# Performance work log

Measured on AMD Instinct MI355X. Metric: run time of the kernel, lower is better.

Reference implementation:

```python
import jax, jax.numpy as jnp
import numpy as np

B, U1, U2 = 4, 2048, 2048
C = 256      # in_feat_dim
F = 256      # feat_dim
M = 4        # num_modes
D = C // M   # attention_mode_dim = 64
ATTN_CLIP = 500.0
LN_EPS = 1e-12


def setup_inputs() -> dict:
    key = jax.random.key(0)
    ks = jax.random.split(key, 8)
    s = 0.02  # base_initializer_range
    inp = {
        "query_feat": jax.random.normal(ks[0], (B, U1, C), jnp.float32),
        "key_feat": jax.random.normal(ks[1], (B, U2, C), jnp.float32),
        "Wq": jax.random.normal(ks[2], (M * D, C), jnp.float32) * s,
        "bq": jnp.zeros((M * D,), jnp.float32),
    }
    # tie_qk_scheme='shared': key linear shares query weights
    inp["Wk"] = inp["Wq"]
    inp["bk"] = inp["bq"]
    inp["Wv"] = jax.random.normal(ks[3], (M * F, C), jnp.float32) * s  # first_linear, v_has_bias=False
    inp["W_mid"] = jax.random.normal(ks[4], (F, F), jnp.float32) * s   # MMSharedMid shared_linear
    inp["b_mid"] = jnp.zeros((F,), jnp.float32)
    inp["W_out"] = jax.random.normal(ks[5], (M, F, F), jnp.float32) * s  # grouped 1x1 conv, per mode
    inp["b_out"] = jnp.zeros((M, F), jnp.float32)
    inp["ln_g"] = jnp.ones((F,), jnp.float32)   # resout LayerNorm
    inp["ln_b"] = jnp.zeros((F,), jnp.float32)
    inp["W_score"] = jax.random.normal(ks[6], (1, F), jnp.float32) * s  # LearnedSoftAggregate
    inp["b_score"] = jnp.zeros((1,), jnp.float32)
    return inp


def _layer_norm(x, g, b):
    mu = jnp.mean(x, axis=-1, keepdims=True)
    var = jnp.var(x, axis=-1, keepdims=True)
    return (x - mu) * jax.lax.rsqrt(var + LN_EPS) * g + b


def reference(query_feat, key_feat, Wq, bq, Wk, bk, Wv, W_mid, b_mid,
              W_out, b_out, ln_g, ln_b, W_score, b_score):
    # --- tied-QK multi-mode attention ---
    q = (query_feat @ Wq.T + bq).reshape(B, U1, M, D)
    k = (key_feat @ Wk.T + bk).reshape(B, U2, M, D)
    scores = jnp.einsum('bimd,bjmd->bmij', q, k) / jnp.sqrt(jnp.float32(D))
    scores = jnp.clip(scores, -ATTN_CLIP, ATTN_CLIP)  # attn_clip
    probs = jax.nn.softmax(scores, axis=-1)           # [B, M, U1, U2]

    # --- ExpandedFeatTrans: value projection + fusion ---
    v = (key_feat @ Wv.T).reshape(B, U2, M, F)        # first_linear (no bias)
    fused = jnp.einsum('bmij,bjmf->bmif', probs, v)   # [B, M, U1, F]

    # MMSharedMid: shared linear over F + gelu (dropout = identity in eval)
    mid = jax.nn.gelu(fused @ W_mid.T + b_mid, approximate=False)

    # MMPrivateOutput: per-mode grouped 1x1 conv; NOTE the original code computes
    # x_comb = x + shortcut but then layer-norms x (shortcut dropped) - kept faithful.
    out = jnp.einsum('bmif,mgf->bmig', mid, W_out) + b_out[None, :, None, :]
    out = _layer_norm(out, ln_g, ln_b)                # [B, M, U1, F]

    # LearnedSoftAggregate over modes (group_dim=1, keepdim=False)
    mode_scores = out @ W_score.T + b_score           # [B, M, U1, 1]
    mode_probs = jax.nn.softmax(mode_scores, axis=1)
    return jnp.sum(out * mode_probs, axis=1)          # [B, U1, F]
```

## Files before the change

kernel.cpp:

```cpp
#include <hip/hip_runtime.h>

typedef __attribute__((ext_vector_type(8))) short short8;
typedef __attribute__((ext_vector_type(4))) float f32x4;
typedef __attribute__((ext_vector_type(16))) float f32x16;
typedef unsigned short u16t;
typedef unsigned int u32t;

#define MFMA16(a, b, c) __builtin_amdgcn_mfma_f32_16x16x32_bf16((a), (b), (c), 0, 0, 0)
#define MFMA32(a, b, c) __builtin_amdgcn_mfma_f32_32x32x16_bf16((a), (b), (c), 0, 0, 0)

__device__ __forceinline__ u16t f2bf(float f) {
  u32t u = __float_as_uint(f);
  u32t r = u + 0x7fffu + ((u >> 16) & 1u);
  return (u16t)(r >> 16);
}
__device__ __forceinline__ float bf2f(u16t b) {
  return __uint_as_float(((u32t)b) << 16);
}
__device__ __forceinline__ short8 pack8(float4 a0, float4 a1) {
  short8 r;
  r[0] = (short)f2bf(a0.x); r[1] = (short)f2bf(a0.y);
  r[2] = (short)f2bf(a0.z); r[3] = (short)f2bf(a0.w);
  r[4] = (short)f2bf(a1.x); r[5] = (short)f2bf(a1.y);
  r[6] = (short)f2bf(a1.z); r[7] = (short)f2bf(a1.w);
  return r;
}
__device__ __forceinline__ u32t packrhu(float a, float b) {
  u32t ua = __float_as_uint(a) + 0x8000u;
  u32t ub = __float_as_uint(b) + 0x8000u;
  return (ua >> 16) | (ub & 0xffff0000u);
}

__device__ __forceinline__ void proj_dev(
    const float* __restrict__ A, const float* __restrict__ W,
    const float* __restrict__ bias, float scale,
    u16t* __restrict__ out, int mode, int bx, int by,
    u16t* As, u16t* Ws) {
  const int tid = threadIdx.x;
  const int w = tid >> 6, lane = tid & 63, quad = lane >> 4, l15 = lane & 15;
  const int l31 = lane & 31, h8 = (lane >> 5) * 8;
  const int rt = bx * 64;
  const int ct = by * 64;
  const int wrow = (w >> 1) * 32, wcol = (w & 1) * 32;
  const int r2 = tid >> 3, c8 = tid & 7;

  const f32x4 fzero = {0.f, 0.f, 0.f, 0.f};
  f32x4 acc[2][2];
#pragma unroll
  for (int i = 0; i < 2; i++)
#pragma unroll
    for (int j = 0; j < 2; j++) acc[i][j] = fzero;

  for (int kt = 0; kt < 4; ++kt) {
    __syncthreads();
#pragma unroll
    for (int hh = 0; hh < 2; ++hh) {
      int rr = r2 + hh * 32;
      const float4* pa = (const float4*)(A + (size_t)(rt + rr) * 256 + kt * 64 + c8 * 8);
      const float4* pw = (const float4*)(W + (size_t)(ct + rr) * 256 + kt * 64 + c8 * 8);
      float4 w0 = pw[0], w1 = pw[1];
      w0.x *= scale; w0.y *= scale; w0.z *= scale; w0.w *= scale;
      w1.x *= scale; w1.y *= scale; w1.z *= scale; w1.w *= scale;
      *(short8*)&As[rr * 72 + c8 * 8] = pack8(pa[0], pa[1]);
      *(short8*)&Ws[rr * 72 + c8 * 8] = pack8(w0, w1);
    }
    __syncthreads();
#pragma unroll
    for (int ks = 0; ks < 2; ++ks) {
      short8 af0 = *(const short8*)&As[(wrow + l15) * 72 + ks * 32 + quad * 8];
      short8 af1 = *(const short8*)&As[(wrow + 16 + l15) * 72 + ks * 32 + quad * 8];
      short8 bw0 = *(const short8*)&Ws[(wcol + l15) * 72 + ks * 32 + quad * 8];
      short8 bw1 = *(const short8*)&Ws[(wcol + 16 + l15) * 72 + ks * 32 + quad * 8];
      acc[0][0] = MFMA16(af0, bw0, acc[0][0]);
      acc[0][1] = MFMA16(af0, bw1, acc[0][1]);
      acc[1][0] = MFMA16(af1, bw0, acc[1][0]);
      acc[1][1] = MFMA16(af1, bw1, acc[1][1]);
    }
  }

  __syncthreads();
  u16t* Cs = As;
  if (mode == 0) {
#pragma unroll
    for (int i = 0; i < 2; i++) {
      int rl = wrow + i * 16 + quad * 4;
#pragma unroll
      for (int j = 0; j < 2; j++) {
        int cl = wcol + j * 16 + l15;
        float bv = bias ? bias[ct + cl] * scale : 0.f;
#pragma unroll
        for (int rg = 0; rg < 4; ++rg)
          Cs[(rl + rg) * 72 + cl] = f2bf(acc[i][j][rg] + bv);
      }
    }
  } else {
#pragma unroll
    for (int i = 0; i < 2; i++) {
      int rl = wrow + i * 16 + quad * 4;
#pragma unroll
      for (int j = 0; j < 2; j++) {
        int cl = wcol + j * 16 + l15;
        ushort4 pk;
        pk.x = f2bf(acc[i][j][0]);
        pk.y = f2bf(acc[i][j][1]);
        pk.z = f2bf(acc[i][j][2]);
        pk.w = f2bf(acc[i][j][3]);
        *(ushort4*)&Cs[cl * 72 + rl] = pk;
      }
    }
  }
  __syncthreads();

#pragma unroll
  for (int t2 = 0; t2 < 2; ++t2) {
    short8 frag = *(const short8*)&Cs[(t2 * 32 + l31) * 72 + w * 16 + h8];
    size_t base;
    if (mode == 0) {
      int b = rt >> 11, m = by;
      int it32 = ((rt & 2047) >> 5) + t2;
      base = (((size_t)(b * 4 + m) * 64 + it32) * 4 + w) * 512;
    } else {
      int b = rt >> 11, m = by >> 2;
      int fb = ((by & 3) << 1) + t2;
      int jt16 = ((rt & 2047) >> 4) + w;
      base = (((size_t)(b * 4 + m) * 8 + fb) * 128 + jt16) * 512;
    }
    *(short8*)(out + base + lane * 8) = frag;
  }
}

__global__ __launch_bounds__(256) void prep_kernel(
    const float* __restrict__ query, const float* __restrict__ key,
    const float* __restrict__ Wq, const float* __restrict__ bq,
    const float* __restrict__ Wv, const float* __restrict__ Wm,
    const float* __restrict__ Wo,
    u16t* __restrict__ WmB, u16t* __restrict__ WoB,
    u16t* __restrict__ QfB, u16t* __restrict__ KfB, u16t* __restrict__ VfB) {
  __shared__ __align__(16) u16t As[64 * 72];
  __shared__ __align__(16) u16t Ws[64 * 72];
  const int blk = blockIdx.x;
  const int tid = threadIdx.x;
  if (blk < 256) {
    int i = blk * 256 + tid;
    WmB[i] = f2bf(Wm[i]);
    return;
  }
  if (blk < 1280) {
    int i = (blk - 256) * 256 + tid;
    WoB[i] = f2bf(Wo[i]);
    return;
  }
  const float *A, *W, *bias;
  float scale;
  u16t* out;
  int mode, local;
  if (blk < 1792) {
    local = blk - 1280; A = query; W = Wq; bias = bq; scale = 0.125f; out = QfB; mode = 0;
  } else if (blk < 2304) {
    local = blk - 1792; A = key; W = Wq; bias = bq; scale = 1.0f; out = KfB; mode = 0;
  } else {
    local = blk - 2304; A = key; W = Wv; bias = nullptr; scale = 1.0f; out = VfB; mode = 1;
  }
  proj_dev(A, W, bias, scale, out, mode, local & 127, local >> 7, As, Ws);
}

__global__ __launch_bounds__(256, 3) void attn_kernel(
    const u16t* __restrict__ Qf, const u16t* __restrict__ Kf,
    const u16t* __restrict__ Vf,
    const u16t* __restrict__ Wmid, const u16t* __restrict__ Wout,
    const float* __restrict__ b_mid, const float* __restrict__ b_out,
    const float* __restrict__ ln_g, const float* __restrict__ ln_b,
    const float* __restrict__ Wsc, const float* __restrict__ b_sc,
    u16t* __restrict__ out_ln, float* __restrict__ scoresWS) {
  __shared__ __align__(16) u16t smF[32 * 264];
  __shared__ __align__(16) u16t smP[2][32 * 132];
  __shared__ float smL[128];
  __shared__ float smR[128];
  __shared__ float smS[64];
  const int tid = threadIdx.x;
  const int w = tid >> 6, lane = tid & 63, quad = lane >> 4, l15 = lane & 15;
  const int l31 = lane & 31, h = lane >> 5;
  const int L = blockIdx.x;
  const int xcd = L & 7, slot = L >> 3;
  const int bm = xcd * 2 + (slot >> 6);
  const int it32 = slot & 63;
  const int m = bm & 3;
  const int q0 = it32 * 32;

  const size_t lane8 = (size_t)lane * 8;

  const u16t* qbase = Qf + ((size_t)(bm * 64 + it32) * 4) * 512 + lane8;
  short8 qf4[4];
#pragma unroll
  for (int ksd = 0; ksd < 4; ++ksd)
    qf4[ksd] = *(const short8*)(qbase + ksd * 512);

  const u16t* kbase = Kf + ((size_t)bm * 256) * 512 + lane8;
  const u16t* vbase = Vf + ((size_t)(bm * 8 + 2 * w) * 128) * 512 + lane8;

  f32x16 facc[2];
#pragma unroll
  for (int j = 0; j < 2; j++)
#pragma unroll
    for (int r = 0; r < 16; r++) facc[j][r] = 0.f;
  float lsum = 0.f;

  short8 kf4[4];
#pragma unroll
  for (int ksd = 0; ksd < 4; ++ksd)
    kf4[ksd] = *(const short8*)(kbase + (size_t)w * 2048 + ksd * 512);

  {
    f32x16 sacc;
#pragma unroll
    for (int r = 0; r < 16; r++) sacc[r] = 0.f;
#pragma unroll
    for (int ksd = 0; ksd < 4; ++ksd)
      sacc = MFMA32(kf4[ksd], qf4[ksd], sacc);
    float ls = 0.f;
#pragma unroll
    for (int tt = 0; tt < 8; ++tt) {
      const int jl = ((2 * tt) & 3) + 8 * ((2 * tt) >> 2) + 4 * h;
      float p0 = __expf(sacc[2 * tt]);
      float p1 = __expf(sacc[2 * tt + 1]);
      ls += p0 + p1;
      *(u32t*)&smP[0][l31 * 132 + w * 32 + jl] = packrhu(p0, p1);
    }
    lsum += ls;
  }
#pragma unroll
  for (int ksd = 0; ksd < 4; ++ksd)
    kf4[ksd] = *(const short8*)(kbase + (size_t)(4 + w) * 2048 + ksd * 512);
  __syncthreads();

#pragma unroll 1
  for (int t = 0; t < 16; ++t) {
    u16t* Pb = &smP[t & 1][0];
    u16t* Pn = &smP[(t + 1) & 1][0];

    if (t < 15) {
      f32x16 sacc;
#pragma unroll
      for (int r = 0; r < 16; r++) sacc[r] = 0.f;
#pragma unroll
      for (int ksd = 0; ksd < 4; ++ksd)
        sacc = MFMA32(kf4[ksd], qf4[ksd], sacc);
      float ls = 0.f;
#pragma unroll
      for (int tt = 0; tt < 8; ++tt) {
        const int jl = ((2 * tt) & 3) + 8 * ((2 * tt) >> 2) + 4 * h;
        float p0 = __expf(sacc[2 * tt]);
        float p1 = __expf(sacc[2 * tt + 1]);
        ls += p0 + p1;
        *(u32t*)&Pn[l31 * 132 + w * 32 + jl] = packrhu(p0, p1);
      }
      lsum += ls;
    }
    if (t < 14) {
      const int jn = (t + 2) * 4 + w;
#pragma unroll
      for (int ksd = 0; ksd < 4; ++ksd)
        kf4[ksd] = *(const short8*)(kbase + (size_t)jn * 2048 + ksd * 512);
    }
#pragma unroll
    for (int jj = 0; jj < 4; ++jj) {
      short8 vf[2][2];
#pragma unroll
      for (int fb = 0; fb < 2; ++fb)
#pragma unroll
        for (int ks2 = 0; ks2 < 2; ++ks2)
          vf[fb][ks2] = *(const short8*)(vbase + ((size_t)fb * 128 + (t * 8 + jj * 2 + ks2)) * 512);
      short8 bbL[2];
#pragma unroll
      for (int ks2 = 0; ks2 < 2; ++ks2)
        bbL[ks2] = *(const short8*)&Pb[l31 * 132 + jj * 32 + ks2 * 16 + h * 8];
      facc[0] = MFMA32(vf[0][0], bbL[0], facc[0]);
      facc[0] = MFMA32(vf[0][1], bbL[1], facc[0]);
      facc[1] = MFMA32(vf[1][0], bbL[0], facc[1]);
      facc[1] = MFMA32(vf[1][1], bbL[1], facc[1]);
    }
    __syncthreads();
  }

  lsum += __shfl_xor(lsum, 32);
  if (h == 0) smL[w * 32 + l31] = lsum;
  __syncthreads();
  float inv = 1.f / (smL[l31] + smL[32 + l31] + smL[64 + l31] + smL[96 + l31]);

#pragma unroll
  for (int fb = 0; fb < 2; ++fb) {
#pragma unroll
    for (int g = 0; g < 4; ++g) {
      int fbase = w * 64 + fb * 32 + 8 * g + 4 * h;
      ushort4 pk4;
      pk4.x = f2bf(facc[fb][4 * g + 0] * inv);
      pk4.y = f2bf(facc[fb][4 * g + 1] * inv);
      pk4.z = f2bf(facc[fb][4 * g + 2] * inv);
      pk4.w = f2bf(facc[fb][4 * g + 3] * inv);
      *(ushort4*)&smF[l31 * 264 + fbase] = pk4;
    }
  }
  __syncthreads();

  const int rgrp = w >> 1, ch = w & 1;
  const int rowq = rgrp * 16 + quad * 4;
  const f32x4 fz4 = {0.f, 0.f, 0.f, 0.f};

  f32x4 macc[8];
#pragma unroll
  for (int i = 0; i < 8; i++) macc[i] = fz4;
  for (int kc = 0; kc < 8; ++kc) {
    short8 af = *(const short8*)&smF[(rgrp * 16 + l15) * 264 + kc * 32 + quad * 8];
#pragma unroll
    for (int nb = 0; nb < 8; ++nb) {
      short8 bw = *(const short8*)(Wmid + (size_t)(ch * 128 + nb * 16 + l15) * 256 + kc * 32 + quad * 8);
      macc[nb] = MFMA16(af, bw, macc[nb]);
    }
  }
#pragma unroll
  for (int nb = 0; nb < 8; ++nb) {
    int c = ch * 128 + nb * 16 + l15;
    float bmv = b_mid[c];
#pragma unroll
    for (int rg = 0; rg < 4; ++rg) {
      float x = macc[nb][rg] + bmv;
      macc[nb][rg] = 0.5f * x * (1.f + erff(x * 0.70710678118654752f));
    }
  }
  __syncthreads();
#pragma unroll
  for (int nb = 0; nb < 8; ++nb)
#pragma unroll
    for (int rg = 0; rg < 4; ++rg)
      smF[(rowq + rg) * 264 + ch * 128 + nb * 16 + l15] = f2bf(macc[nb][rg]);
  __syncthreads();

  const u16t* Wo = Wout + (size_t)m * 65536;
  f32x4 oacc[8];
#pragma unroll
  for (int i = 0; i < 8; i++) oacc[i] = fz4;
  for (int kc = 0; kc < 8; ++kc) {
    short8 af = *(const short8*)&smF[(rgrp * 16 + l15) * 264 + kc * 32 + quad * 8];
#pragma unroll
    for (int nb = 0; nb < 8; ++nb) {
      short8 bw = *(const short8*)(Wo + (size_t)(ch * 128 + nb * 16 + l15) * 256 + kc * 32 + quad * 8);
      oacc[nb] = MFMA16(af, bw, oacc[nb]);
    }
  }

  float sum[4] = {0, 0, 0, 0}, sq[4] = {0, 0, 0, 0};
#pragma unroll
  for (int nb = 0; nb < 8; ++nb) {
    int c = ch * 128 + nb * 16 + l15;
    float bo = b_out[m * 256 + c];
#pragma unroll
    for (int rg = 0; rg < 4; ++rg) {
      float x = oacc[nb][rg] + bo;
      oacc[nb][rg] = x;
      sum[rg] += x;
      sq[rg] += x * x;
    }
  }
#pragma unroll
  for (int rg = 0; rg < 4; ++rg) {
    float s = sum[rg], s2 = sq[rg];
    s += __shfl_xor(s, 1); s += __shfl_xor(s, 2); s += __shfl_xor(s, 4); s += __shfl_xor(s, 8);
    s2 += __shfl_xor(s2, 1); s2 += __shfl_xor(s2, 2); s2 += __shfl_xor(s2, 4); s2 += __shfl_xor(s2, 8);
    if (l15 == 0) {
      smR[(rowq + rg) + 32 * ch] = s;
      smR[64 + (rowq + rg) + 32 * ch] = s2;
    }
  }
  __syncthreads();
  float mu[4], rstd[4];
#pragma unroll
  for (int rg = 0; rg < 4; ++rg) {
    int r = rowq + rg;
    float s = smR[r] + smR[r + 32];
    float s2 = smR[64 + r] + smR[64 + r + 32];
    float mean = s * (1.f / 256.f);
    float var = s2 * (1.f / 256.f) - mean * mean;
    mu[rg] = mean;
    rstd[rg] = rsqrtf(var + 1e-12f);
  }

  float scp[4] = {0, 0, 0, 0};
#pragma unroll
  for (int nb = 0; nb < 8; ++nb) {
    int c = ch * 128 + nb * 16 + l15;
    float g = ln_g[c], bb2 = ln_b[c], wsv = Wsc[c];
#pragma unroll
    for (int rg = 0; rg < 4; ++rg) {
      float xn = (oacc[nb][rg] - mu[rg]) * rstd[rg] * g + bb2;
      out_ln[((size_t)bm * 2048 + (q0 + rowq + rg)) * 256 + c] = f2bf(xn);
      scp[rg] += xn * wsv;
    }
  }
#pragma unroll
  for (int rg = 0; rg < 4; ++rg) {
    float s = scp[rg];
    s += __shfl_xor(s, 1); s += __shfl_xor(s, 2); s += __shfl_xor(s, 4); s += __shfl_xor(s, 8);
    if (l15 == 0) smS[(rowq + rg) + 32 * ch] = s;
  }
  __syncthreads();
  if (ch == 0 && l15 == 0) {
#pragma unroll
    for (int rg = 0; rg < 4; ++rg) {
      int r = rowq + rg;
      scoresWS[bm * 2048 + q0 + r] = smS[r] + smS[r + 32] + b_sc[0];
    }
  }
}

__global__ __launch_bounds__(256) void agg_kernel(
    const u16t* __restrict__ out_ln, const float* __restrict__ scoresWS,
    float* __restrict__ out) {
  const int row = blockIdx.x;
  const int c = threadIdx.x;
  const int b = row >> 11, i = row & 2047;
  float s0 = scoresWS[(b * 4 + 0) * 2048 + i];
  float s1 = scoresWS[(b * 4 + 1) * 2048 + i];
  float s2 = scoresWS[(b * 4 + 2) * 2048 + i];
  float s3 = scoresWS[(b * 4 + 3) * 2048 + i];
  float mx = fmaxf(fmaxf(s0, s1), fmaxf(s2, s3));
  float e0 = __expf(s0 - mx), e1 = __expf(s1 - mx), e2 = __expf(s2 - mx), e3 = __expf(s3 - mx);
  float inv = 1.f / (e0 + e1 + e2 + e3);
  float acc = e0 * inv * bf2f(out_ln[((size_t)(b * 4 + 0) * 2048 + i) * 256 + c]) +
              e1 * inv * bf2f(out_ln[((size_t)(b * 4 + 1) * 2048 + i) * 256 + c]) +
              e2 * inv * bf2f(out_ln[((size_t)(b * 4 + 2) * 2048 + i) * 256 + c]) +
              e3 * inv * bf2f(out_ln[((size_t)(b * 4 + 3) * 2048 + i) * 256 + c]);
  out[(size_t)row * 256 + c] = acc;
}

extern "C" void kernel_launch(void* const* d_in, const int* in_sizes, int n_in,
                              void* d_out, int out_size, void* d_ws, size_t ws_size,
                              hipStream_t stream) {
  (void)in_sizes; (void)n_in; (void)out_size; (void)ws_size;
  const float* query = (const float*)d_in[0];
  const float* key   = (const float*)d_in[1];
  const float* Wq    = (const float*)d_in[2];
  const float* bq    = (const float*)d_in[3];
  const float* Wv    = (const float*)d_in[6];
  const float* Wm    = (const float*)d_in[7];
  const float* bmid  = (const float*)d_in[8];
  const float* Wo    = (const float*)d_in[9];
  const float* bo    = (const float*)d_in[10];
  const float* lng   = (const float*)d_in[11];
  const float* lnb   = (const float*)d_in[12];
  const float* Wsc   = (const float*)d_in[13];
  const float* bsc   = (const float*)d_in[14];

  char* p = (char*)d_ws;
  u16t* QfB = (u16t*)p; p += (size_t)2097152 * 2;
  u16t* KfB = (u16t*)p; p += (size_t)2097152 * 2;
  u16t* VfB = (u16t*)p; p += (size_t)8388608 * 2;
  u16t* WmB = (u16t*)p; p += (size_t)65536 * 2;
  u16t* WoB = (u16t*)p; p += (size_t)262144 * 2;
  u16t* outLn = (u16t*)p; p += (size_t)8388608 * 2;
  float* scWS = (float*)p; p += (size_t)32768 * 4;

  prep_kernel<<<4352, 256, 0, stream>>>(query, key, Wq, bq, Wv, Wm, Wo,
                                        WmB, WoB, QfB, KfB, VfB);

  attn_kernel<<<1024, 256, 0, stream>>>(QfB, KfB, VfB, WmB, WoB,
                                        bmid, bo, lng, lnb, Wsc, bsc,
                                        outLn, scWS);

  agg_kernel<<<8192, 256, 0, stream>>>(outLn, scWS, (float*)d_out);
}
```

Measured before the change: 237.3 us.

## Double query tile per block to 64 rows with 8 waves sharing V loads

The attention kernel now processes 64 query rows per block with 512 threads (8 waves) instead of 32 rows with 256 threads. Each V fragment loaded from global memory is reused across two 32-row halves of the probability tile, halving V traffic per query row. Shared memory and reduction arrays double, and the grid halves. The cost is fewer blocks, more shared memory per block, and a changed occupancy target that may limit latency hiding.

```diff
diff --git a/kernel.cpp b/kernel.cpp
--- a/kernel.cpp
+++ b/kernel.cpp
@@ -164,7 +164,7 @@
   proj_dev(A, W, bias, scale, out, mode, local & 127, local >> 7, As, Ws);
 }
 
-__global__ __launch_bounds__(256, 3) void attn_kernel(
+__global__ __launch_bounds__(512, 4) void attn_kernel(
     const u16t* __restrict__ Qf, const u16t* __restrict__ Kf,
     const u16t* __restrict__ Vf,
     const u16t* __restrict__ Wmid, const u16t* __restrict__ Wout,
@@ -172,31 +172,32 @@
     const float* __restrict__ ln_g, const float* __restrict__ ln_b,
     const float* __restrict__ Wsc, const float* __restrict__ b_sc,
     u16t* __restrict__ out_ln, float* __restrict__ scoresWS) {
-  __shared__ __align__(16) u16t smF[32 * 264];
-  __shared__ __align__(16) u16t smP[2][32 * 132];
-  __shared__ float smL[128];
-  __shared__ float smR[128];
-  __shared__ float smS[64];
+  __shared__ __align__(16) u16t smF[64 * 264];
+  __shared__ __align__(16) u16t smP[2][64 * 132];
+  __shared__ float smL[256];
+  __shared__ float smR[256];
+  __shared__ float smS[128];
   const int tid = threadIdx.x;
   const int w = tid >> 6, lane = tid & 63, quad = lane >> 4, l15 = lane & 15;
   const int l31 = lane & 31, h = lane >> 5;
   const int L = blockIdx.x;
   const int xcd = L & 7, slot = L >> 3;
-  const int bm = xcd * 2 + (slot >> 6);
-  const int it32 = slot & 63;
+  const int bm = xcd * 2 + (slot >> 5);
+  const int it64 = slot & 31;
   const int m = bm & 3;
-  const int q0 = it32 * 32;
+  const int q0 = it64 * 64;
+  const int jw = w & 3, ihS = w >> 2;
 
   const size_t lane8 = (size_t)lane * 8;
 
-  const u16t* qbase = Qf + ((size_t)(bm * 64 + it32) * 4) * 512 + lane8;
+  const u16t* qbase = Qf + ((size_t)(bm * 64 + it64 * 2 + ihS) * 4) * 512 + lane8;
   short8 qf4[4];
 #pragma unroll
   for (int ksd = 0; ksd < 4; ++ksd)
     qf4[ksd] = *(const short8*)(qbase + ksd * 512);
 
   const u16t* kbase = Kf + ((size_t)bm * 256) * 512 + lane8;
-  const u16t* vbase = Vf + ((size_t)(bm * 8 + 2 * w) * 128) * 512 + lane8;
+  const u16t* vbase = Vf + ((size_t)(bm * 8 + w) * 128) * 512 + lane8;
 
   f32x16 facc[2];
 #pragma unroll
@@ -208,7 +209,7 @@
   short8 kf4[4];
 #pragma unroll
   for (int ksd = 0; ksd < 4; ++ksd)
-    kf4[ksd] = *(const short8*)(kbase + (size_t)w * 2048 + ksd * 512);
+    kf4[ksd] = *(const short8*)(kbase + (size_t)jw * 2048 + ksd * 512);
 
   {
     f32x16 sacc;
@@ -224,13 +225,13 @@
       float p0 = __expf(sacc[2 * tt]);
       float p1 = __expf(sacc[2 * tt + 1]);
       ls += p0 + p1;
-      *(u32t*)&smP[0][l31 * 132 + w * 32 + jl] = packrhu(p0, p1);
+      *(u32t*)&smP[0][(ihS * 32 + l31) * 132 + jw * 32 + jl] = packrhu(p0, p1);
     }
     lsum += ls;
   }
 #pragma unroll
   for (int ksd = 0; ksd < 4; ++ksd)
-    kf4[ksd] = *(const short8*)(kbase + (size_t)(4 + w) * 2048 + ksd * 512);
+    kf4[ksd] = *(const short8*)(kbase + (size_t)(4 + jw) * 2048 + ksd * 512);
   __syncthreads();
 
 #pragma unroll 1
@@ -252,32 +253,23 @@
         float p0 = __expf(sacc[2 * tt]);
         float p1 = __expf(sacc[2 * tt + 1]);
         ls += p0 + p1;
-        *(u32t*)&Pn[l31 * 132 + w * 32 + jl] = packrhu(p0, p1);
+        *(u32t*)&Pn[(ihS * 32 + l31) * 132 + jw * 32 + jl] = packrhu(p0, p1);
       }
       lsum += ls;
     }
     if (t < 14) {
-      const int jn = (t + 2) * 4 + w;
+      const int jn = (t + 2) * 4 + jw;
 #pragma unroll
       for (int ksd = 0; ksd < 4; ++ksd)
         kf4[ksd] = *(const short8*)(kbase + (size_t)jn * 2048 + ksd * 512);
     }
 #pragma unroll
-    for (int jj = 0; jj < 4; ++jj) {
-      short8 vf[2][2];
-#pragma unroll
-      for (int fb = 0; fb < 2; ++fb)
-#pragma unroll
-        for (int ks2 = 0; ks2 < 2; ++ks2)
-          vf[fb][ks2] = *(const short8*)(vbase + ((size_t)fb * 128 + (t * 8 + jj * 2 + ks2)) * 512);
-      short8 bbL[2];
-#pragma unroll
-      for (int ks2 = 0; ks2 < 2; ++ks2)
-        bbL[ks2] = *(const short8*)&Pb[l31 * 132 + jj * 32 + ks2 * 16 + h * 8];
-      facc[0] = MFMA32(vf[0][0], bbL[0], facc[0]);
-      facc[0] = MFMA32(vf[0][1], bbL[1], facc[0]);
-      facc[1] = MFMA32(vf[1][0], bbL[0], facc[1]);
-      facc[1] = MFMA32(vf[1][1], bbL[1], facc[1]);
+    for (int ks = 0; ks < 8; ++ks) {
+      short8 vf = *(const short8*)(vbase + ((size_t)(t * 8 + ks)) * 512);
+      short8 b0 = *(const short8*)&Pb[l31 * 132 + ks * 16 + h * 8];
+      short8 b1 = *(const short8*)&Pb[(32 + l31) * 132 + ks * 16 + h * 8];
+      facc[0] = MFMA32(vf, b0, facc[0]);
+      facc[1] = MFMA32(vf, b1, facc[1]);
     }
     __syncthreads();
   }
@@ -285,19 +277,23 @@
   lsum += __shfl_xor(lsum, 32);
   if (h == 0) smL[w * 32 + l31] = lsum;
   __syncthreads();
-  float inv = 1.f / (smL[l31] + smL[32 + l31] + smL[64 + l31] + smL[96 + l31]);
-
-#pragma unroll
-  for (int fb = 0; fb < 2; ++fb) {
+  float inv[2];
+#pragma unroll
+  for (int ih = 0; ih < 2; ++ih)
+    inv[ih] = 1.f / (smL[(ih * 4 + 0) * 32 + l31] + smL[(ih * 4 + 1) * 32 + l31] +
+                     smL[(ih * 4 + 2) * 32 + l31] + smL[(ih * 4 + 3) * 32 + l31]);
+
+#pragma unroll
+  for (int ih = 0; ih < 2; ++ih) {
 #pragma unroll
     for (int g = 0; g < 4; ++g) {
-      int fbase = w * 64 + fb * 32 + 8 * g + 4 * h;
+      int fbase = w * 32 + 8 * g + 4 * h;
       ushort4 pk4;
-      pk4.x = f2bf(facc[fb][4 * g + 0] * inv);
-      pk4.y = f2bf(facc[fb][4 * g + 1] * inv);
-      pk4.z = f2bf(facc[fb][4 * g + 2] * inv);
-      pk4.w = f2bf(facc[fb][4 * g + 3] * inv);
-      *(ushort4*)&smF[l31 * 264 + fbase] = pk4;
+      pk4.x = f2bf(facc[ih][4 * g + 0] * inv[ih]);
+      pk4.y = f2bf(facc[ih][4 * g + 1] * inv[ih]);
+      pk4.z = f2bf(facc[ih][4 * g + 2] * inv[ih]);
+      pk4.w = f2bf(facc[ih][4 * g + 3] * inv[ih]);
+      *(ushort4*)&smF[(ih * 32 + l31) * 264 + fbase] = pk4;
     }
   }
   __syncthreads();
@@ -367,8 +363,8 @@
     s += __shfl_xor(s, 1); s += __shfl_xor(s, 2); s += __shfl_xor(s, 4); s += __shfl_xor(s, 8);
     s2 += __shfl_xor(s2, 1); s2 += __shfl_xor(s2, 2); s2 += __shfl_xor(s2, 4); s2 += __shfl_xor(s2, 8);
     if (l15 == 0) {
-      smR[(rowq + rg) + 32 * ch] = s;
-      smR[64 + (rowq + rg) + 32 * ch] = s2;
+      smR[(rowq + rg) + 64 * ch] = s;
+      smR[128 + (rowq + rg) + 64 * ch] = s2;
     }
   }
   __syncthreads();
@@ -376,8 +372,8 @@
 #pragma unroll
   for (int rg = 0; rg < 4; ++rg) {
     int r = rowq + rg;
-    float s = smR[r] + smR[r + 32];
-    float s2 = smR[64 + r] + smR[64 + r + 32];
+    float s = smR[r] + smR[r + 64];
+    float s2 = smR[128 + r] + smR[128 + r + 64];
     float mean = s * (1.f / 256.f);
     float var = s2 * (1.f / 256.f) - mean * mean;
     mu[rg] = mean;
@@ -400,14 +396,14 @@
   for (int rg = 0; rg < 4; ++rg) {
     float s = scp[rg];
     s += __shfl_xor(s, 1); s += __shfl_xor(s, 2); s += __shfl_xor(s, 4); s += __shfl_xor(s, 8);
-    if (l15 == 0) smS[(rowq + rg) + 32 * ch] = s;
+    if (l15 == 0) smS[(rowq + rg) + 64 * ch] = s;
   }
   __syncthreads();
   if (ch == 0 && l15 == 0) {
 #pragma unroll
     for (int rg = 0; rg < 4; ++rg) {
       int r = rowq + rg;
-      scoresWS[bm * 2048 + q0 + r] = smS[r] + smS[r + 32] + b_sc[0];
+      scoresWS[bm * 2048 + q0 + r] = smS[r] + smS[r + 64] + b_sc[0];
     }
   }
 }
@@ -462,9 +458,9 @@
   prep_kernel<<<4352, 256, 0, stream>>>(query, key, Wq, bq, Wv, Wm, Wo,
                                         WmB, WoB, QfB, KfB, VfB);
 
-  attn_kernel<<<1024, 256, 0, stream>>>(QfB, KfB, VfB, WmB, WoB,
-                                        bmid, bo, lng, lnb, Wsc, bsc,
-                                        outLn, scWS);
+  attn_kernel<<<512, 512, 0, stream>>>(QfB, KfB, VfB, WmB, WoB,
+                                       bmid, bo, lng, lnb, Wsc, bsc,
+                                       outLn, scWS);
 
   agg_kernel<<<8192, 256, 0, stream>>>(outLn, scWS, (float*)d_out);
 }
```

After: 281.8 us. 18.7% more time.

## Split weight conversion into own kernel and widen projection tiles to reuse activations

Applied to the files above, without the earlier changes.

Weight-to-bf16 conversion moves into a separate vectorized cvt kernel. The projection kernel now reads activation fragments straight from global memory into registers and reuses them across four 64-column output blocks, each block covering 256 columns. This cuts redundant activation loads and fp32-to-bf16 conversions and drops LDS staging in the main loop. It adds a kernel launch and more accumulator registers, and the attention kernel's launch bounds are raised to allow 4 blocks per CU.

```diff
diff --git a/kernel.cpp b/kernel.cpp
--- a/kernel.cpp
+++ b/kernel.cpp
@@ -31,140 +31,142 @@
   return (ua >> 16) | (ub & 0xffff0000u);
 }
 
-__device__ __forceinline__ void proj_dev(
-    const float* __restrict__ A, const float* __restrict__ W,
-    const float* __restrict__ bias, float scale,
-    u16t* __restrict__ out, int mode, int bx, int by,
-    u16t* As, u16t* Ws) {
+__global__ __launch_bounds__(256) void cvt_kernel(
+    const float* __restrict__ Wq, const float* __restrict__ Wv,
+    const float* __restrict__ Wm, const float* __restrict__ Wo,
+    u16t* __restrict__ WqB, u16t* __restrict__ WvB,
+    u16t* __restrict__ WmB, u16t* __restrict__ WoB) {
+  const int blk = blockIdx.x, tid = threadIdx.x;
+  const float* src; u16t* dst; int base;
+  if (blk < 64)       { src = Wq; dst = WqB; base = blk * 1024; }
+  else if (blk < 320) { src = Wv; dst = WvB; base = (blk - 64) * 1024; }
+  else if (blk < 384) { src = Wm; dst = WmB; base = (blk - 320) * 1024; }
+  else                { src = Wo; dst = WoB; base = (blk - 384) * 1024; }
+  int i = base + tid * 4;
+  float4 v = *(const float4*)(src + i);
+  ushort4 o;
+  o.x = f2bf(v.x); o.y = f2bf(v.y); o.z = f2bf(v.z); o.w = f2bf(v.w);
+  *(ushort4*)(dst + i) = o;
+}
+
+__global__ __launch_bounds__(256, 4) void proj_kernel(
+    const float* __restrict__ query, const float* __restrict__ key,
+    const u16t* __restrict__ WqB, const u16t* __restrict__ WvB,
+    const float* __restrict__ bq,
+    u16t* __restrict__ QfB, u16t* __restrict__ KfB, u16t* __restrict__ VfB) {
+  __shared__ __align__(16) u16t Cs[64 * 72];
   const int tid = threadIdx.x;
   const int w = tid >> 6, lane = tid & 63, quad = lane >> 4, l15 = lane & 15;
   const int l31 = lane & 31, h8 = (lane >> 5) * 8;
+  const int wrow = (w >> 1) * 32, wcol = (w & 1) * 32;
+
+  const float* A; const u16t* W16; const float* bias;
+  float ascale; u16t* out; int mode, bx, byg;
+  const int blk = blockIdx.x;
+  if (blk < 128) {
+    A = query; W16 = WqB; bias = bq; ascale = 0.125f; out = QfB; mode = 0; bx = blk; byg = 0;
+  } else if (blk < 256) {
+    A = key; W16 = WqB; bias = bq; ascale = 1.0f; out = KfB; mode = 0; bx = blk - 128; byg = 0;
+  } else {
+    int v2 = blk - 256;
+    A = key; W16 = WvB; bias = nullptr; ascale = 1.0f; out = VfB; mode = 1;
+    bx = v2 & 127; byg = v2 >> 7;
+  }
   const int rt = bx * 64;
-  const int ct = by * 64;
-  const int wrow = (w >> 1) * 32, wcol = (w & 1) * 32;
-  const int r2 = tid >> 3, c8 = tid & 7;
-
-  const f32x4 fzero = {0.f, 0.f, 0.f, 0.f};
-  f32x4 acc[2][2];
-#pragma unroll
-  for (int i = 0; i < 2; i++)
-#pragma unroll
-    for (int j = 0; j < 2; j++) acc[i][j] = fzero;
-
-  for (int kt = 0; kt < 4; ++kt) {
+
+  const f32x4 fz = {0.f, 0.f, 0.f, 0.f};
+  f32x4 acc[4][2][2];
+#pragma unroll
+  for (int n = 0; n < 4; n++)
+#pragma unroll
+    for (int i = 0; i < 2; i++)
+#pragma unroll
+      for (int j = 0; j < 2; j++) acc[n][i][j] = fz;
+
+  const float* arow0 = A + (size_t)(rt + wrow + l15) * 256;
+  const float* arow1 = A + (size_t)(rt + wrow + 16 + l15) * 256;
+  const u16t* wbase = W16 + (size_t)(byg * 256 + wcol + l15) * 256;
+
+#pragma unroll
+  for (int ks = 0; ks < 8; ++ks) {
+    const int kk = ks * 32 + quad * 8;
+    float4 a00 = *(const float4*)(arow0 + kk);
+    float4 a01 = *(const float4*)(arow0 + kk + 4);
+    float4 a10 = *(const float4*)(arow1 + kk);
+    float4 a11 = *(const float4*)(arow1 + kk + 4);
+    a00.x *= ascale; a00.y *= ascale; a00.z *= ascale; a00.w *= ascale;
+    a01.x *= ascale; a01.y *= ascale; a01.z *= ascale; a01.w *= ascale;
+    a10.x *= ascale; a10.y *= ascale; a10.z *= ascale; a10.w *= ascale;
+    a11.x *= ascale; a11.y *= ascale; a11.z *= ascale; a11.w *= ascale;
+    short8 af0 = pack8(a00, a01);
+    short8 af1 = pack8(a10, a11);
+#pragma unroll
+    for (int nby = 0; nby < 4; ++nby) {
+      const u16t* wb = wbase + (size_t)nby * 64 * 256 + kk;
+      short8 bw0 = *(const short8*)(wb);
+      short8 bw1 = *(const short8*)(wb + 16 * 256);
+      acc[nby][0][0] = MFMA16(af0, bw0, acc[nby][0][0]);
+      acc[nby][0][1] = MFMA16(af0, bw1, acc[nby][0][1]);
+      acc[nby][1][0] = MFMA16(af1, bw0, acc[nby][1][0]);
+      acc[nby][1][1] = MFMA16(af1, bw1, acc[nby][1][1]);
+    }
+  }
+
+#pragma unroll 1
+  for (int nby = 0; nby < 4; ++nby) {
+    const int by = byg * 4 + nby;
+    const int ct = by * 64;
     __syncthreads();
-#pragma unroll
-    for (int hh = 0; hh < 2; ++hh) {
-      int rr = r2 + hh * 32;
-      const float4* pa = (const float4*)(A + (size_t)(rt + rr) * 256 + kt * 64 + c8 * 8);
-      const float4* pw = (const float4*)(W + (size_t)(ct + rr) * 256 + kt * 64 + c8 * 8);
-      float4 w0 = pw[0], w1 = pw[1];
-      w0.x *= scale; w0.y *= scale; w0.z *= scale; w0.w *= scale;
-      w1.x *= scale; w1.y *= scale; w1.z *= scale; w1.w *= scale;
-      *(short8*)&As[rr * 72 + c8 * 8] = pack8(pa[0], pa[1]);
-      *(short8*)&Ws[rr * 72 + c8 * 8] = pack8(w0, w1);
+    if (mode == 0) {
+#pragma unroll
+      for (int i = 0; i < 2; i++) {
+        int rl = wrow + i * 16 + quad * 4;
+#pragma unroll
+        for (int j = 0; j < 2; j++) {
+          int cl = wcol + j * 16 + l15;
+          float bv = bias ? bias[ct + cl] * ascale : 0.f;
+#pragma unroll
+          for (int rg = 0; rg < 4; ++rg)
+            Cs[(rl + rg) * 72 + cl] = f2bf(acc[nby][i][j][rg] + bv);
+        }
+      }
+    } else {
+#pragma unroll
+      for (int i = 0; i < 2; i++) {
+        int rl = wrow + i * 16 + quad * 4;
+#pragma unroll
+        for (int j = 0; j < 2; j++) {
+          int cl = wcol + j * 16 + l15;
+          ushort4 pk;
+          pk.x = f2bf(acc[nby][i][j][0]);
+          pk.y = f2bf(acc[nby][i][j][1]);
+          pk.z = f2bf(acc[nby][i][j][2]);
+          pk.w = f2bf(acc[nby][i][j][3]);
+          *(ushort4*)&Cs[cl * 72 + rl] = pk;
+        }
+      }
     }
     __syncthreads();
 #pragma unroll
-    for (int ks = 0; ks < 2; ++ks) {
-      short8 af0 = *(const short8*)&As[(wrow + l15) * 72 + ks * 32 + quad * 8];
-      short8 af1 = *(const short8*)&As[(wrow + 16 + l15) * 72 + ks * 32 + quad * 8];
-      short8 bw0 = *(const short8*)&Ws[(wcol + l15) * 72 + ks * 32 + quad * 8];
-      short8 bw1 = *(const short8*)&Ws[(wcol + 16 + l15) * 72 + ks * 32 + quad * 8];
-      acc[0][0] = MFMA16(af0, bw0, acc[0][0]);
-      acc[0][1] = MFMA16(af0, bw1, acc[0][1]);
-      acc[1][0] = MFMA16(af1, bw0, acc[1][0]);
-      acc[1][1] = MFMA16(af1, bw1, acc[1][1]);
-    }
-  }
-
-  __syncthreads();
-  u16t* Cs = As;
-  if (mode == 0) {
-#pragma unroll
-    for (int i = 0; i < 2; i++) {
-      int rl = wrow + i * 16 + quad * 4;
-#pragma unroll
-      for (int j = 0; j < 2; j++) {
-        int cl = wcol + j * 16 + l15;
-        float bv = bias ? bias[ct + cl] * scale : 0.f;
-#pragma unroll
-        for (int rg = 0; rg < 4; ++rg)
-          Cs[(rl + rg) * 72 + cl] = f2bf(acc[i][j][rg] + bv);
+    for (int t2 = 0; t2 < 2; ++t2) {
+      short8 frag = *(const short8*)&Cs[(t2 * 32 + l31) * 72 + w * 16 + h8];
+      size_t base;
+      if (mode == 0) {
+        int b = rt >> 11, m = by;
+        int it32 = ((rt & 2047) >> 5) + t2;
+        base = (((size_t)(b * 4 + m) * 64 + it32) * 4 + w) * 512;
+      } else {
+        int b = rt >> 11, m = by >> 2;
+        int fb = ((by & 3) << 1) + t2;
+        int jt16 = ((rt & 2047) >> 4) + w;
+        base = (((size_t)(b * 4 + m) * 8 + fb) * 128 + jt16) * 512;
       }
-    }
-  } else {
-#pragma unroll
-    for (int i = 0; i < 2; i++) {
-      int rl = wrow + i * 16 + quad * 4;
-#pragma unroll
-      for (int j = 0; j < 2; j++) {
-        int cl = wcol + j * 16 + l15;
-        ushort4 pk;
-        pk.x = f2bf(acc[i][j][0]);
-        pk.y = f2bf(acc[i][j][1]);
-        pk.z = f2bf(acc[i][j][2]);
-        pk.w = f2bf(acc[i][j][3]);
-        *(ushort4*)&Cs[cl * 72 + rl] = pk;
-      }
-    }
-  }
-  __syncthreads();
-
-#pragma unroll
-  for (int t2 = 0; t2 < 2; ++t2) {
-    short8 frag = *(const short8*)&Cs[(t2 * 32 + l31) * 72 + w * 16 + h8];
-    size_t base;
-    if (mode == 0) {
-      int b = rt >> 11, m = by;
-      int it32 = ((rt & 2047) >> 5) + t2;
-      base = (((size_t)(b * 4 + m) * 64 + it32) * 4 + w) * 512;
-    } else {
-      int b = rt >> 11, m = by >> 2;
-      int fb = ((by & 3) << 1) + t2;
-      int jt16 = ((rt & 2047) >> 4) + w;
-      base = (((size_t)(b * 4 + m) * 8 + fb) * 128 + jt16) * 512;
-    }
-    *(short8*)(out + base + lane * 8) = frag;
-  }
-}
-
-__global__ __launch_bounds__(256) void prep_kernel(
-    const float* __restrict__ query, const float* __restrict__ key,
-    const float* __restrict__ Wq, const float* __restrict__ bq,
-    const float* __restrict__ Wv, const float* __restrict__ Wm,
-    const float* __restrict__ Wo,
-    u16t* __restrict__ WmB, u16t* __restrict__ WoB,
-    u16t* __restrict__ QfB, u16t* __restrict__ KfB, u16t* __restrict__ VfB) {
-  __shared__ __align__(16) u16t As[64 * 72];
-  __shared__ __align__(16) u16t Ws[64 * 72];
-  const int blk = blockIdx.x;
-  const int tid = threadIdx.x;
-  if (blk < 256) {
-    int i = blk * 256 + tid;
-    WmB[i] = f2bf(Wm[i]);
-    return;
-  }
-  if (blk < 1280) {
-    int i = (blk - 256) * 256 + tid;
-    WoB[i] = f2bf(Wo[i]);
-    return;
-  }
-  const float *A, *W, *bias;
-  float scale;
-  u16t* out;
-  int mode, local;
-  if (blk < 1792) {
-    local = blk - 1280; A = query; W = Wq; bias = bq; scale = 0.125f; out = QfB; mode = 0;
-  } else if (blk < 2304) {
-    local = blk - 1792; A = key; W = Wq; bias = bq; scale = 1.0f; out = KfB; mode = 0;
-  } else {
-    local = blk - 2304; A = key; W = Wv; bias = nullptr; scale = 1.0f; out = VfB; mode = 1;
-  }
-  proj_dev(A, W, bias, scale, out, mode, local & 127, local >> 7, As, Ws);
-}
-
-__global__ __launch_bounds__(256, 3) void attn_kernel(
+      *(short8*)(out + base + lane * 8) = frag;
+    }
+  }
+}
+
+__global__ __launch_bounds__(256, 4) void attn_kernel(
     const u16t* __restrict__ Qf, const u16t* __restrict__ Kf,
     const u16t* __restrict__ Vf,
     const u16t* __restrict__ Wmid, const u16t* __restrict__ Wout,
@@ -456,11 +458,15 @@
   u16t* VfB = (u16t*)p; p += (size_t)8388608 * 2;
   u16t* WmB = (u16t*)p; p += (size_t)65536 * 2;
   u16t* WoB = (u16t*)p; p += (size_t)262144 * 2;
+  u16t* WqB = (u16t*)p; p += (size_t)65536 * 2;
+  u16t* WvB = (u16t*)p; p += (size_t)262144 * 2;
   u16t* outLn = (u16t*)p; p += (size_t)8388608 * 2;
   float* scWS = (float*)p; p += (size_t)32768 * 4;
 
-  prep_kernel<<<4352, 256, 0, stream>>>(query, key, Wq, bq, Wv, Wm, Wo,
-                                        WmB, WoB, QfB, KfB, VfB);
+  cvt_kernel<<<640, 256, 0, stream>>>(Wq, Wv, Wm, Wo, WqB, WvB, WmB, WoB);
+
+  proj_kernel<<<768, 256, 0, stream>>>(query, key, WqB, WvB, bq,
+                                       QfB, KfB, VfB);
 
   attn_kernel<<<1024, 256, 0, stream>>>(QfB, KfB, VfB, WmB, WoB,
                                         bmid, bo, lng, lnb, Wsc, bsc,
```

Result: slower. 277.7 us (+17.0%).

## Reuse converted input tile across output tiles in projection and alias attention LDS

Applied to the files above, without the earlier changes.

The projection prep kernel now loads and converts each 64-row activation tile to bf16 once, keeping it in LDS and registers. Each block then loops over four 64-column weight tiles, cutting redundant global reads and conversions of query and key. The weight-conversion blocks are vectorized to four elements per thread, which shrinks the grid. The attention kernel aliases its fused-feature buffer with the double-buffered probability buffer and raises launch bounds from 3 to 4 blocks per CU, trading register headroom for occupancy.

```diff
diff --git a/kernel.cpp b/kernel.cpp
--- a/kernel.cpp
+++ b/kernel.cpp
@@ -31,104 +31,6 @@
   return (ua >> 16) | (ub & 0xffff0000u);
 }
 
-__device__ __forceinline__ void proj_dev(
-    const float* __restrict__ A, const float* __restrict__ W,
-    const float* __restrict__ bias, float scale,
-    u16t* __restrict__ out, int mode, int bx, int by,
-    u16t* As, u16t* Ws) {
-  const int tid = threadIdx.x;
-  const int w = tid >> 6, lane = tid & 63, quad = lane >> 4, l15 = lane & 15;
-  const int l31 = lane & 31, h8 = (lane >> 5) * 8;
-  const int rt = bx * 64;
-  const int ct = by * 64;
-  const int wrow = (w >> 1) * 32, wcol = (w & 1) * 32;
-  const int r2 = tid >> 3, c8 = tid & 7;
-
-  const f32x4 fzero = {0.f, 0.f, 0.f, 0.f};
-  f32x4 acc[2][2];
-#pragma unroll
-  for (int i = 0; i < 2; i++)
-#pragma unroll
-    for (int j = 0; j < 2; j++) acc[i][j] = fzero;
-
-  for (int kt = 0; kt < 4; ++kt) {
-    __syncthreads();
-#pragma unroll
-    for (int hh = 0; hh < 2; ++hh) {
-      int rr = r2 + hh * 32;
-      const float4* pa = (const float4*)(A + (size_t)(rt + rr) * 256 + kt * 64 + c8 * 8);
-      const float4* pw = (const float4*)(W + (size_t)(ct + rr) * 256 + kt * 64 + c8 * 8);
-      float4 w0 = pw[0], w1 = pw[1];
-      w0.x *= scale; w0.y *= scale; w0.z *= scale; w0.w *= scale;
-      w1.x *= scale; w1.y *= scale; w1.z *= scale; w1.w *= scale;
-      *(short8*)&As[rr * 72 + c8 * 8] = pack8(pa[0], pa[1]);
-      *(short8*)&Ws[rr * 72 + c8 * 8] = pack8(w0, w1);
-    }
-    __syncthreads();
-#pragma unroll
-    for (int ks = 0; ks < 2; ++ks) {
-      short8 af0 = *(const short8*)&As[(wrow + l15) * 72 + ks * 32 + quad * 8];
-      short8 af1 = *(const short8*)&As[(wrow + 16 + l15) * 72 + ks * 32 + quad * 8];
-      short8 bw0 = *(const short8*)&Ws[(wcol + l15) * 72 + ks * 32 + quad * 8];
-      short8 bw1 = *(const short8*)&Ws[(wcol + 16 + l15) * 72 + ks * 32 + quad * 8];
-      acc[0][0] = MFMA16(af0, bw0, acc[0][0]);
-      acc[0][1] = MFMA16(af0, bw1, acc[0][1]);
-      acc[1][0] = MFMA16(af1, bw0, acc[1][0]);
-      acc[1][1] = MFMA16(af1, bw1, acc[1][1]);
-    }
-  }
-
-  __syncthreads();
-  u16t* Cs = As;
-  if (mode == 0) {
-#pragma unroll
-    for (int i = 0; i < 2; i++) {
-      int rl = wrow + i * 16 + quad * 4;
-#pragma unroll
-      for (int j = 0; j < 2; j++) {
-        int cl = wcol + j * 16 + l15;
-        float bv = bias ? bias[ct + cl] * scale : 0.f;
-#pragma unroll
-        for (int rg = 0; rg < 4; ++rg)
-          Cs[(rl + rg) * 72 + cl] = f2bf(acc[i][j][rg] + bv);
-      }
-    }
-  } else {
-#pragma unroll
-    for (int i = 0; i < 2; i++) {
-      int rl = wrow + i * 16 + quad * 4;
-#pragma unroll
-      for (int j = 0; j < 2; j++) {
-        int cl = wcol + j * 16 + l15;
-        ushort4 pk;
-        pk.x = f2bf(acc[i][j][0]);
-        pk.y = f2bf(acc[i][j][1]);
-        pk.z = f2bf(acc[i][j][2]);
-        pk.w = f2bf(acc[i][j][3]);
-        *(ushort4*)&Cs[cl * 72 + rl] = pk;
-      }
-    }
-  }
-  __syncthreads();
-
-#pragma unroll
-  for (int t2 = 0; t2 < 2; ++t2) {
-    short8 frag = *(const short8*)&Cs[(t2 * 32 + l31) * 72 + w * 16 + h8];
-    size_t base;
-    if (mode == 0) {
-      int b = rt >> 11, m = by;
-      int it32 = ((rt & 2047) >> 5) + t2;
-      base = (((size_t)(b * 4 + m) * 64 + it32) * 4 + w) * 512;
-    } else {
-      int b = rt >> 11, m = by >> 2;
-      int fb = ((by & 3) << 1) + t2;
-      int jt16 = ((rt & 2047) >> 4) + w;
-      base = (((size_t)(b * 4 + m) * 8 + fb) * 128 + jt16) * 512;
-    }
-    *(short8*)(out + base + lane * 8) = frag;
-  }
-}
-
 __global__ __launch_bounds__(256) void prep_kernel(
     const float* __restrict__ query, const float* __restrict__ key,
     const float* __restrict__ Wq, const float* __restrict__ bq,
@@ -136,35 +38,150 @@
     const float* __restrict__ Wo,
     u16t* __restrict__ WmB, u16t* __restrict__ WoB,
     u16t* __restrict__ QfB, u16t* __restrict__ KfB, u16t* __restrict__ VfB) {
-  __shared__ __align__(16) u16t As[64 * 72];
-  __shared__ __align__(16) u16t Ws[64 * 72];
   const int blk = blockIdx.x;
   const int tid = threadIdx.x;
-  if (blk < 256) {
-    int i = blk * 256 + tid;
-    WmB[i] = f2bf(Wm[i]);
+
+  if (blk >= 768) {
+    int cv = blk - 768;
+    const float* src; u16t* dst; int base;
+    if (cv < 64) { src = Wm; dst = WmB; base = cv * 1024; }
+    else         { src = Wo; dst = WoB; base = (cv - 64) * 1024; }
+    int i = base + tid * 4;
+    float4 v = *(const float4*)(src + i);
+    ushort4 o2;
+    o2.x = f2bf(v.x); o2.y = f2bf(v.y); o2.z = f2bf(v.z); o2.w = f2bf(v.w);
+    *(ushort4*)(dst + i) = o2;
     return;
   }
-  if (blk < 1280) {
-    int i = (blk - 256) * 256 + tid;
-    WoB[i] = f2bf(Wo[i]);
-    return;
-  }
-  const float *A, *W, *bias;
-  float scale;
-  u16t* out;
-  int mode, local;
-  if (blk < 1792) {
-    local = blk - 1280; A = query; W = Wq; bias = bq; scale = 0.125f; out = QfB; mode = 0;
-  } else if (blk < 2304) {
-    local = blk - 1792; A = key; W = Wq; bias = bq; scale = 1.0f; out = KfB; mode = 0;
+
+  __shared__ __align__(16) u16t As[64 * 264];
+  __shared__ __align__(16) u16t Ws[64 * 72];
+
+  const int w = tid >> 6, lane = tid & 63, quad = lane >> 4, l15 = lane & 15;
+  const int l31 = lane & 31, h8 = (lane >> 5) * 8;
+  const int wrow = (w >> 1) * 32, wcol = (w & 1) * 32;
+  const int r2 = tid >> 3, c8 = tid & 7;
+
+  const float* A; const float* W; const float* bias;
+  float scale; u16t* outp; int mode, bx, by0;
+  if (blk < 128) {
+    A = query; W = Wq; bias = bq; scale = 0.125f; outp = QfB; mode = 0; bx = blk; by0 = 0;
+  } else if (blk < 256) {
+    A = key; W = Wq; bias = bq; scale = 1.0f; outp = KfB; mode = 0; bx = blk - 128; by0 = 0;
   } else {
-    local = blk - 2304; A = key; W = Wv; bias = nullptr; scale = 1.0f; out = VfB; mode = 1;
-  }
-  proj_dev(A, W, bias, scale, out, mode, local & 127, local >> 7, As, Ws);
-}
-
-__global__ __launch_bounds__(256, 3) void attn_kernel(
+    int v2 = blk - 256;
+    A = key; W = Wv; bias = nullptr; scale = 1.0f; outp = VfB; mode = 1;
+    bx = v2 & 127; by0 = (v2 >> 7) * 4;
+  }
+  const int rt = bx * 64;
+
+#pragma unroll
+  for (int hh = 0; hh < 2; ++hh) {
+    int rr = r2 + hh * 32;
+    const float* arow = A + (size_t)(rt + rr) * 256;
+#pragma unroll
+    for (int kt = 0; kt < 4; ++kt) {
+      const float4* pa = (const float4*)(arow + kt * 64 + c8 * 8);
+      float4 a0 = pa[0], a1 = pa[1];
+      a0.x *= scale; a0.y *= scale; a0.z *= scale; a0.w *= scale;
+      a1.x *= scale; a1.y *= scale; a1.z *= scale; a1.w *= scale;
+      *(short8*)&As[rr * 264 + kt * 64 + c8 * 8] = pack8(a0, a1);
+    }
+  }
+  __syncthreads();
+
+  short8 af[8][2];
+#pragma unroll
+  for (int ks8 = 0; ks8 < 8; ++ks8) {
+    af[ks8][0] = *(const short8*)&As[(wrow + l15) * 264 + ks8 * 32 + quad * 8];
+    af[ks8][1] = *(const short8*)&As[(wrow + 16 + l15) * 264 + ks8 * 32 + quad * 8];
+  }
+
+#pragma unroll 1
+  for (int nt = 0; nt < 4; ++nt) {
+    const int by = by0 + nt;
+    const int ct = by * 64;
+
+    const f32x4 fz = {0.f, 0.f, 0.f, 0.f};
+    f32x4 acc[2][2];
+#pragma unroll
+    for (int i = 0; i < 2; i++)
+#pragma unroll
+      for (int j = 0; j < 2; j++) acc[i][j] = fz;
+
+#pragma unroll
+    for (int kt = 0; kt < 4; ++kt) {
+      __syncthreads();
+#pragma unroll
+      for (int hh = 0; hh < 2; ++hh) {
+        int rr = r2 + hh * 32;
+        const float4* pw = (const float4*)(W + (size_t)(ct + rr) * 256 + kt * 64 + c8 * 8);
+        *(short8*)&Ws[rr * 72 + c8 * 8] = pack8(pw[0], pw[1]);
+      }
+      __syncthreads();
+#pragma unroll
+      for (int ks = 0; ks < 2; ++ks) {
+        short8 bw0 = *(const short8*)&Ws[(wcol + l15) * 72 + ks * 32 + quad * 8];
+        short8 bw1 = *(const short8*)&Ws[(wcol + 16 + l15) * 72 + ks * 32 + quad * 8];
+        acc[0][0] = MFMA16(af[kt * 2 + ks][0], bw0, acc[0][0]);
+        acc[0][1] = MFMA16(af[kt * 2 + ks][0], bw1, acc[0][1]);
+        acc[1][0] = MFMA16(af[kt * 2 + ks][1], bw0, acc[1][0]);
+        acc[1][1] = MFMA16(af[kt * 2 + ks][1], bw1, acc[1][1]);
+      }
+    }
+
+    __syncthreads();
+    u16t* Cs = Ws;
+    if (mode == 0) {
+#pragma unroll
+      for (int i = 0; i < 2; i++) {
+        int rl = wrow + i * 16 + quad * 4;
+#pragma unroll
+        for (int j = 0; j < 2; j++) {
+          int cl = wcol + j * 16 + l15;
+          float bv = bias ? bias[ct + cl] * scale : 0.f;
+#pragma unroll
+          for (int rg = 0; rg < 4; ++rg)
+            Cs[(rl + rg) * 72 + cl] = f2bf(acc[i][j][rg] + bv);
+        }
+      }
+    } else {
+#pragma unroll
+      for (int i = 0; i < 2; i++) {
+        int rl = wrow + i * 16 + quad * 4;
+#pragma unroll
+        for (int j = 0; j < 2; j++) {
+          int cl = wcol + j * 16 + l15;
+          ushort4 pk;
+          pk.x = f2bf(acc[i][j][0]);
+          pk.y = f2bf(acc[i][j][1]);
+          pk.z = f2bf(acc[i][j][2]);
+          pk.w = f2bf(acc[i][j][3]);
+          *(ushort4*)&Cs[cl * 72 + rl] = pk;
+        }
+      }
+    }
+    __syncthreads();
+#pragma unroll
+    for (int t2 = 0; t2 < 2; ++t2) {
+      short8 frag = *(const short8*)&Cs[(t2 * 32 + l31) * 72 + w * 16 + h8];
+      size_t base;
+      if (mode == 0) {
+        int b = rt >> 11, m = by;
+        int it32 = ((rt & 2047) >> 5) + t2;
+        base = (((size_t)(b * 4 + m) * 64 + it32) * 4 + w) * 512;
+      } else {
+        int b = rt >> 11, m = by >> 2;
+        int fb = ((by & 3) << 1) + t2;
+        int jt16 = ((rt & 2047) >> 4) + w;
+        base = (((size_t)(b * 4 + m) * 8 + fb) * 128 + jt16) * 512;
+      }
+      *(short8*)(outp + base + lane * 8) = frag;
+    }
+  }
+}
+
+__global__ __launch_bounds__(256, 4) void attn_kernel(
     const u16t* __restrict__ Qf, const u16t* __restrict__ Kf,
     const u16t* __restrict__ Vf,
     const u16t* __restrict__ Wmid, const u16t* __restrict__ Wout,
@@ -172,8 +189,7 @@
     const float* __restrict__ ln_g, const float* __restrict__ ln_b,
     const float* __restrict__ Wsc, const float* __restrict__ b_sc,
     u16t* __restrict__ out_ln, float* __restrict__ scoresWS) {
-  __shared__ __align__(16) u16t smF[32 * 264];
-  __shared__ __align__(16) u16t smP[2][32 * 132];
+  __shared__ __align__(16) u16t smU[8448];
   __shared__ float smL[128];
   __shared__ float smR[128];
   __shared__ float smS[64];
@@ -224,7 +240,7 @@
       float p0 = __expf(sacc[2 * tt]);
       float p1 = __expf(sacc[2 * tt + 1]);
       ls += p0 + p1;
-      *(u32t*)&smP[0][l31 * 132 + w * 32 + jl] = packrhu(p0, p1);
+      *(u32t*)&smU[l31 * 132 + w * 32 + jl] = packrhu(p0, p1);
     }
     lsum += ls;
   }
@@ -235,8 +251,8 @@
 
 #pragma unroll 1
   for (int t = 0; t < 16; ++t) {
-    u16t* Pb = &smP[t & 1][0];
-    u16t* Pn = &smP[(t + 1) & 1][0];
+    u16t* Pb = (t & 1) ? smU + 4224 : smU;
+    u16t* Pn = (t & 1) ? smU : smU + 4224;
 
     if (t < 15) {
       f32x16 sacc;
@@ -287,6 +303,7 @@
   __syncthreads();
   float inv = 1.f / (smL[l31] + smL[32 + l31] + smL[64 + l31] + smL[96 + l31]);
 
+  u16t* const smF = smU;
 #pragma unroll
   for (int fb = 0; fb < 2; ++fb) {
 #pragma unroll
@@ -459,7 +476,7 @@
   u16t* outLn = (u16t*)p; p += (size_t)8388608 * 2;
   float* scWS = (float*)p; p += (size_t)32768 * 4;
 
-  prep_kernel<<<4352, 256, 0, stream>>>(query, key, Wq, bq, Wv, Wm, Wo,
+  prep_kernel<<<1088, 256, 0, stream>>>(query, key, Wq, bq, Wv, Wm, Wo,
                                         WmB, WoB, QfB, KfB, VfB);
 
   attn_kernel<<<1024, 256, 0, stream>>>(QfB, KfB, VfB, WmB, WoB,
```

After: 236.7 us. No clear change (-0.2%).
